# Optimization experiments

Hardware: AMD Instinct MI355X
Metric: run time of the kernel (lower is better)

Reference implementation:

```python
import jax, jax.numpy as jnp
import numpy as np

N_SRC, N_DST, N_EDGE, D = 100000, 40000, 600000, 128
LN_EPS = 1e-5

def _mlp(x, w1, b1, w2, b2, g, beta):
    # anemoi MLP: Linear -> SiLU -> Linear -> LayerNorm
    h = jax.nn.silu(x @ w1 + b1)
    h = h @ w2 + b2
    mu = jnp.mean(h, axis=-1, keepdims=True)
    var = jnp.var(h, axis=-1, keepdims=True)
    return (h - mu) * jax.lax.rsqrt(var + LN_EPS) * g + beta

def setup_inputs() -> dict:
    key = jax.random.key(0)
    ks = jax.random.split(key, 12)
    def rn(k, shape, scale):
        return jax.random.normal(k, shape, dtype=jnp.float32) * scale
    w_scale = 0.05
    return dict(
        x_src=rn(ks[0], (N_SRC, D), 1.0),
        x_dst=rn(ks[1], (N_DST, D), 1.0),
        edge_attr=rn(ks[2], (N_EDGE, D), 1.0),
        edge_index=jnp.stack([
            jax.random.randint(ks[3], (N_EDGE,), 0, N_SRC),
            jax.random.randint(ks[4], (N_EDGE,), 0, N_DST)]).astype(jnp.int32),
        edge_w1=rn(ks[5], (3 * D, D), w_scale), edge_b1=jnp.zeros((D,), jnp.float32),
        edge_w2=rn(ks[6], (D, D), w_scale), edge_b2=jnp.zeros((D,), jnp.float32),
        edge_g=jnp.ones((D,), jnp.float32), edge_beta=jnp.zeros((D,), jnp.float32),
        node_w1=rn(ks[7], (2 * D, D), w_scale), node_b1=jnp.zeros((D,), jnp.float32),
        node_w2=rn(ks[8], (D, D), w_scale), node_b2=jnp.zeros((D,), jnp.float32),
        node_g=jnp.ones((D,), jnp.float32), node_beta=jnp.zeros((D,), jnp.float32),
    )

def reference(x_src, x_dst, edge_attr, edge_index,
              edge_w1, edge_b1, edge_w2, edge_b2, edge_g, edge_beta,
              node_w1, node_b1, node_w2, node_b2, node_g, node_beta):
    src, dst = edge_index[0], edge_index[1]
    # GraphConv message: x_i = dst node feats, x_j = src node feats (PyG source_to_target)
    x_i = x_dst[dst]              # [E, D] gather
    x_j = x_src[src]              # [E, D] gather
    edges_new = _mlp(jnp.concatenate([x_i, x_j, edge_attr], axis=-1),
                     edge_w1, edge_b1, edge_w2, edge_b2, edge_g, edge_beta) + edge_attr
    # sum-aggregate messages to dst nodes (chunked sum == single sum)
    agg = jax.ops.segment_sum(edges_new, dst, num_segments=N_DST)  # [N_DST, D]
    nodes_new_dst = _mlp(jnp.concatenate([x_dst, agg], axis=-1),
                         node_w1, node_b1, node_w2, node_b2, node_g, node_beta) + x_dst
    # update_src_nodes=True branch
    nodes_new_src = _mlp(jnp.concatenate([x_src, x_src], axis=-1),
                         node_w1, node_b1, node_w2, node_b2, node_g, node_beta) + x_src
    return nodes_new_src, nodes_new_dst, edges_new
```

## Files before the change

### kernel.cpp

```cpp
#include <hip/hip_runtime.h>
#include <hip/hip_bf16.h>

#define NSRC  100000
#define NDST  40000
#define NEDGE 600000
#define AGG_BYTES   20480000ull
#define GB_BYTES    2048ull
#define W1F_OFF   (AGG_BYTES + GB_BYTES)
#define W2F_OFF   (W1F_OFF + 98304ull)
#define NW1F_OFF  (W2F_OFF + 32768ull)
#define NW2F_OFF  (NW1F_OFF + 65536ull)
#define NW1SF_OFF (NW2F_OFF + 32768ull)
#define WS_REQUIRED (NW1SF_OFF + 32768ull)

typedef __bf16 bf16;
typedef __attribute__((ext_vector_type(8))) __bf16 bf16x8;
typedef __attribute__((ext_vector_type(4))) float f32x4;

__device__ __forceinline__ unsigned short bfbits(float f) {
    return __builtin_bit_cast(unsigned short, (__bf16)f);
}

__device__ __forceinline__ f32x4 mfma16(bf16x8 a, bf16x8 b, f32x4 c) {
    return __builtin_amdgcn_mfma_f32_16x16x32_bf16(a, b, c, 0, 0, 0);
}

__device__ __forceinline__ bf16x8 pack8(float4 a, float4 b) {
    union { uint4 u; bf16x8 v; } o;
    o.u.x = (unsigned)bfbits(a.x) | ((unsigned)bfbits(a.y) << 16);
    o.u.y = (unsigned)bfbits(a.z) | ((unsigned)bfbits(a.w) << 16);
    o.u.z = (unsigned)bfbits(b.x) | ((unsigned)bfbits(b.y) << 16);
    o.u.w = (unsigned)bfbits(b.z) | ((unsigned)bfbits(b.w) << 16);
    return o.v;
}

__device__ __forceinline__ bf16x8 cvt8p(const float* p) {
    return pack8(*(const float4*)p, *(const float4*)(p + 4));
}

__device__ __forceinline__ void cvt8hl(const float* p, bf16x8& hi, bf16x8& lo) {
    float4 a = *(const float4*)p;
    float4 b = *(const float4*)(p + 4);
    float v[8] = {a.x, a.y, a.z, a.w, b.x, b.y, b.z, b.w};
    union { uint4 u; bf16x8 v; } H, L;
    unsigned hw[8], lw[8];
#pragma unroll
    for (int i = 0; i < 8; ++i) {
        bf16 h = (bf16)v[i];
        hw[i] = (unsigned)__builtin_bit_cast(unsigned short, h);
        lw[i] = (unsigned)bfbits(v[i] - (float)h);
    }
    H.u.x = hw[0] | (hw[1] << 16); H.u.y = hw[2] | (hw[3] << 16);
    H.u.z = hw[4] | (hw[5] << 16); H.u.w = hw[6] | (hw[7] << 16);
    L.u.x = lw[0] | (lw[1] << 16); L.u.y = lw[2] | (lw[3] << 16);
    L.u.z = lw[4] | (lw[5] << 16); L.u.w = lw[6] | (lw[7] << 16);
    hi = H.v; lo = L.v;
}

__global__ __launch_bounds__(256) void prep_kernel(
    const float* __restrict__ w1, const float* __restrict__ w2,
    const float* __restrict__ nw1, const float* __restrict__ nw2,
    bf16* __restrict__ w1f, bf16* __restrict__ w2f,
    bf16* __restrict__ nw1f, bf16* __restrict__ nw2f, bf16* __restrict__ nw1sf) {
    int i = blockIdx.x * 256 + threadIdx.x;
    if (i < 49152) {
        int j = i & 7, lane = (i >> 3) & 63, f = (i >> 9) & 3;
        int rest = i >> 11; int ks = rest % 12, wc = rest / 12;
        int k = ks * 32 + (lane >> 4) * 8 + j;
        int n = wc * 64 + f * 16 + (lane & 15);
        w1f[i] = (bf16)w1[k * 128 + n];
    } else if (i < 65536) {
        int q = i - 49152;
        int j = q & 7, lane = (q >> 3) & 63, f = (q >> 9) & 3;
        int rest = q >> 11; int ks = rest & 3, wc = rest >> 2;
        int k = ks * 32 + (lane >> 4) * 8 + j;
        int n = wc * 64 + f * 16 + (lane & 15);
        w2f[q] = (bf16)w2[k * 128 + n];
    } else if (i < 98304) {
        int q = i - 65536;
        int j = q & 7, lane = (q >> 3) & 63, f = (q >> 9) & 3;
        int rest = q >> 11; int ks = rest & 7, wc = rest >> 3;
        int k = ks * 32 + (lane >> 4) * 8 + j;
        int n = wc * 64 + f * 16 + (lane & 15);
        nw1f[q] = (bf16)nw1[k * 128 + n];
    } else if (i < 114688) {
        int q = i - 98304;
        int j = q & 7, lane = (q >> 3) & 63, f = (q >> 9) & 3;
        int rest = q >> 11; int ks = rest & 3, wc = rest >> 2;
        int k = ks * 32 + (lane >> 4) * 8 + j;
        int n = wc * 64 + f * 16 + (lane & 15);
        nw2f[q] = (bf16)nw2[k * 128 + n];
    } else {
        int q = i - 114688;
        int j = q & 7, lane = (q >> 3) & 63, f = (q >> 9) & 3;
        int rest = q >> 11; int ks = rest & 3, wc = rest >> 2;
        int k = ks * 32 + (lane >> 4) * 8 + j;
        int n = wc * 64 + f * 16 + (lane & 15);
        nw1sf[q] = (bf16)(nw1[k * 128 + n] + nw1[(k + 128) * 128 + n]);
    }
}

__global__ void select_gbeta(const float* __restrict__ a, const float* __restrict__ b,
                             float* __restrict__ g_out, float* __restrict__ beta_out) {
    int t = threadIdx.x;
    bool a_is_g = (a[0] == 1.0f);
    const float* g  = a_is_g ? a : b;
    const float* be = a_is_g ? b : a;
    g_out[t]    = g[t];
    beta_out[t] = be[t];
}

__device__ __forceinline__ void mlp_tail(
    f32x4 (&acc)[2][4], char* sH, float* redS, float* redQ,
    const bf16x8* w2v, const float* b1, const float* b2,
    const float* g, const float* be,
    int wr, int wc, int lr, int lg, int lane,
    float (&outv)[2][4][4])
{
    {
        float b1c[4];
#pragma unroll
        for (int fc = 0; fc < 4; ++fc) b1c[fc] = b1[wc * 64 + fc * 16 + lr];
#pragma unroll
        for (int fr = 0; fr < 2; ++fr)
#pragma unroll
            for (int fc = 0; fc < 4; ++fc)
#pragma unroll
                for (int rg = 0; rg < 4; ++rg) {
                    int row = wr * 32 + fr * 16 + lg * 4 + rg;
                    int col = wc * 64 + fc * 16 + lr;
                    float v = acc[fr][fc][rg] + b1c[fc];
                    v = v / (1.f + __expf(-v));
                    *(bf16*)(sH + ((row * 256 + col * 2) ^ ((row & 7) << 4))) = (bf16)v;
                }
    }
    __syncthreads();

#pragma unroll
    for (int i = 0; i < 2; ++i)
#pragma unroll
        for (int j = 0; j < 4; ++j) acc[i][j] = f32x4{0.f, 0.f, 0.f, 0.f};
#pragma unroll
    for (int ks = 0; ks < 4; ++ks) {
        bf16x8 a[2], b[4];
#pragma unroll
        for (int f = 0; f < 2; ++f) {
            int ra = wr * 32 + f * 16 + lr;
            a[f] = *(const bf16x8*)(sH + ((ra * 256 + ks * 64 + lg * 16) ^ ((ra & 7) << 4)));
        }
#pragma unroll
        for (int fc = 0; fc < 4; ++fc)
            b[fc] = w2v[((wc * 4 + ks) * 4 + fc) * 64 + lane];
#pragma unroll
        for (int i = 0; i < 2; ++i)
#pragma unroll
            for (int j = 0; j < 4; ++j)
                acc[i][j] = mfma16(a[i], b[j], acc[i][j]);
    }

    float b2c[4], gc[4], bc[4];
#pragma unroll
    for (int fc = 0; fc < 4; ++fc) {
        int col = wc * 64 + fc * 16 + lr;
        b2c[fc] = b2[col]; gc[fc] = g[col]; bc[fc] = be[col];
    }
#pragma unroll
    for (int fr = 0; fr < 2; ++fr)
#pragma unroll
        for (int rg = 0; rg < 4; ++rg) {
            float s = 0.f, sq = 0.f;
#pragma unroll
            for (int fc = 0; fc < 4; ++fc) {
                float v = acc[fr][fc][rg] + b2c[fc];
                acc[fr][fc][rg] = v;
                s += v; sq += v * v;
            }
#pragma unroll
            for (int m = 1; m < 16; m <<= 1) {
                s  += __shfl_xor(s, m, 64);
                sq += __shfl_xor(sq, m, 64);
            }
            if (lr == 0) {
                int row = wr * 32 + fr * 16 + lg * 4 + rg;
                redS[row * 2 + wc] = s;
                redQ[row * 2 + wc] = sq;
            }
        }
    __syncthreads();

#pragma unroll
    for (int fr = 0; fr < 2; ++fr)
#pragma unroll
        for (int rg = 0; rg < 4; ++rg) {
            int row = wr * 32 + fr * 16 + lg * 4 + rg;
            float s  = redS[row * 2] + redS[row * 2 + 1];
            float sq = redQ[row * 2] + redQ[row * 2 + 1];
            float mean = s * (1.f / 128.f);
            float var  = fmaxf(sq * (1.f / 128.f) - mean * mean, 0.f);
            float rstd = rsqrtf(var + 1e-5f);
#pragma unroll
            for (int fc = 0; fc < 4; ++fc)
                outv[fr][fc][rg] = (acc[fr][fc][rg] - mean) * rstd * gc[fc] + bc[fc];
        }
}

__global__ __launch_bounds__(256, 4) void edge_mfma(
    const float* __restrict__ xsrc, const float* __restrict__ xdst,
    const float* __restrict__ attr, const int* __restrict__ eidx,
    const bf16* __restrict__ w1f,  const bf16* __restrict__ w2f,
    const float* __restrict__ b1,  const float* __restrict__ b2,
    const float* __restrict__ g,   const float* __restrict__ be,
    float* __restrict__ oute, float* __restrict__ agg)
{
    __shared__ __align__(16) char sH[16384];
    __shared__ float redS[128], redQ[128];
    __shared__ int sS[64], sD[64];

    const int t = threadIdx.x;
    const long e0 = (long)blockIdx.x * 64;
    if (t < 64) {
        long e = e0 + t;
        sS[t] = min(max(eidx[e], 0), NSRC - 1);
        sD[t] = min(max(eidx[NEDGE + e], 0), NDST - 1);
    }
    __syncthreads();

    const int lane = t & 63, w = t >> 6;
    const int wr = w >> 1, wc = w & 1;
    const int lr = lane & 15, lg = lane >> 4;

    const int r0w = wr * 32 + lr, r1w = r0w + 16;
    const float* xi0 = xdst + (long)sD[r0w] * 128;
    const float* xi1 = xdst + (long)sD[r1w] * 128;
    const float* xj0 = xsrc + (long)sS[r0w] * 128;
    const float* xj1 = xsrc + (long)sS[r1w] * 128;
    const float* at0 = attr + (e0 + r0w) * 128;
    const float* at1 = attr + (e0 + r1w) * 128;

    const bf16x8* w1v = (const bf16x8*)w1f;
    const bf16x8* w2v = (const bf16x8*)w2f;

    f32x4 acc[2][4];
#pragma unroll
    for (int i = 0; i < 2; ++i)
#pragma unroll
        for (int j = 0; j < 4; ++j) acc[i][j] = f32x4{0.f, 0.f, 0.f, 0.f};

    float4 raw[3][2][2];
#define LOADKS(d_, ks_) { \
        const float* q0 = ((ks_) < 4 ? xi0 : (ks_) < 8 ? xj0 : at0) + (((ks_) & 3) * 32 + lg * 8); \
        const float* q1 = ((ks_) < 4 ? xi1 : (ks_) < 8 ? xj1 : at1) + (((ks_) & 3) * 32 + lg * 8); \
        raw[d_][0][0] = *(const float4*)q0; raw[d_][0][1] = *(const float4*)(q0 + 4); \
        raw[d_][1][0] = *(const float4*)q1; raw[d_][1][1] = *(const float4*)(q1 + 4); }

    LOADKS(0, 0) LOADKS(1, 1) LOADKS(2, 2)

#pragma unroll
    for (int ks = 0; ks < 12; ++ks) {
        const int d = ks % 3;
        bf16x8 a0 = pack8(raw[d][0][0], raw[d][0][1]);
        bf16x8 a1 = pack8(raw[d][1][0], raw[d][1][1]);
        if (ks + 3 < 12) { LOADKS(d, ks + 3) }
        bf16x8 b[4];
#pragma unroll
        for (int fc = 0; fc < 4; ++fc)
            b[fc] = w1v[((wc * 12 + ks) * 4 + fc) * 64 + lane];
#pragma unroll
        for (int j = 0; j < 4; ++j) {
            acc[0][j] = mfma16(a0, b[j], acc[0][j]);
            acc[1][j] = mfma16(a1, b[j], acc[1][j]);
        }
    }
#undef LOADKS

    float outv[2][4][4];
    mlp_tail(acc, sH, redS, redQ, w2v, b1, b2, g, be, wr, wc, lr, lg, lane, outv);

#pragma unroll
    for (int fr = 0; fr < 2; ++fr)
#pragma unroll
        for (int rg = 0; rg < 4; ++rg) {
            int row = wr * 32 + fr * 16 + lg * 4 + rg;
            long e = e0 + row;
            long dbase = (long)sD[row] * 128;
#pragma unroll
            for (int fc = 0; fc < 4; ++fc) {
                int col = wc * 64 + fc * 16 + lr;
                float v = outv[fr][fc][rg] + attr[e * 128 + col];
                __builtin_nontemporal_store(v, &oute[e * 128 + col]);
                atomicAdd(agg + dbase + col, v);
            }
        }
}

__global__ __launch_bounds__(256, 4) void node_src_mfma(
    const float* __restrict__ xsrc,
    const bf16* __restrict__ nw1sf, const bf16* __restrict__ nw2f,
    const float* __restrict__ b1, const float* __restrict__ b2,
    const float* __restrict__ g,  const float* __restrict__ be,
    float* __restrict__ outp)
{
    __shared__ __align__(16) char sH[16384];
    __shared__ float redS[128], redQ[128];

    const int t = threadIdx.x;
    const long r0 = (long)blockIdx.x * 64;
    const int lane = t & 63, w = t >> 6;
    const int wr = w >> 1, wc = w & 1;
    const int lr = lane & 15, lg = lane >> 4;

    long gr0 = r0 + wr * 32 + lr;      if (gr0 >= NSRC) gr0 = NSRC - 1;
    long gr1 = r0 + wr * 32 + 16 + lr; if (gr1 >= NSRC) gr1 = NSRC - 1;
    const float* x0 = xsrc + gr0 * 128;
    const float* x1 = xsrc + gr1 * 128;

    const bf16x8* w1v = (const bf16x8*)nw1sf;
    const bf16x8* w2v = (const bf16x8*)nw2f;

    f32x4 acc[2][4];
#pragma unroll
    for (int i = 0; i < 2; ++i)
#pragma unroll
        for (int j = 0; j < 4; ++j) acc[i][j] = f32x4{0.f, 0.f, 0.f, 0.f};

#pragma unroll
    for (int ks = 0; ks < 4; ++ks) {
        int k0 = ks * 32 + lg * 8;
        bf16x8 a0 = cvt8p(x0 + k0);
        bf16x8 a1 = cvt8p(x1 + k0);
        bf16x8 b[4];
#pragma unroll
        for (int fc = 0; fc < 4; ++fc)
            b[fc] = w1v[((wc * 4 + ks) * 4 + fc) * 64 + lane];
#pragma unroll
        for (int j = 0; j < 4; ++j) {
            acc[0][j] = mfma16(a0, b[j], acc[0][j]);
            acc[1][j] = mfma16(a1, b[j], acc[1][j]);
        }
    }

    float outv[2][4][4];
    mlp_tail(acc, sH, redS, redQ, w2v, b1, b2, g, be, wr, wc, lr, lg, lane, outv);

#pragma unroll
    for (int fr = 0; fr < 2; ++fr)
#pragma unroll
        for (int rg = 0; rg < 4; ++rg) {
            int row = wr * 32 + fr * 16 + lg * 4 + rg;
            long gr = r0 + row;
            if (gr < NSRC) {
#pragma unroll
                for (int fc = 0; fc < 4; ++fc) {
                    int col = wc * 64 + fc * 16 + lr;
                    float v = outv[fr][fc][rg] + xsrc[gr * 128 + col];
                    __builtin_nontemporal_store(v, &outp[gr * 128 + col]);
                }
            }
        }
}

__global__ __launch_bounds__(256, 4) void node_dst_mfma(
    const float* __restrict__ xdst, const float* __restrict__ agg,
    const bf16* __restrict__ nw1f, const bf16* __restrict__ nw2f,
    const float* __restrict__ b1, const float* __restrict__ b2,
    const float* __restrict__ g,  const float* __restrict__ be,
    float* __restrict__ outp)
{
    __shared__ __align__(16) char sH[16384];
    __shared__ float redS[128], redQ[128];

    const int t = threadIdx.x;
    const long r0 = (long)blockIdx.x * 64;
    const int lane = t & 63, w = t >> 6;
    const int wr = w >> 1, wc = w & 1;
    const int lr = lane & 15, lg = lane >> 4;

    long gr0 = r0 + wr * 32 + lr;
    long gr1 = gr0 + 16;
    const float* x0 = xdst + gr0 * 128;
    const float* x1 = xdst + gr1 * 128;
    const float* a0p = agg + gr0 * 128;
    const float* a1p = agg + gr1 * 128;

    const bf16x8* w1v = (const bf16x8*)nw1f;
    const bf16x8* w2v = (const bf16x8*)nw2f;

    f32x4 acc[2][4];
#pragma unroll
    for (int i = 0; i < 2; ++i)
#pragma unroll
        for (int j = 0; j < 4; ++j) acc[i][j] = f32x4{0.f, 0.f, 0.f, 0.f};

#pragma unroll
    for (int ks = 0; ks < 4; ++ks) {
        int k0 = ks * 32 + lg * 8;
        bf16x8 a0 = cvt8p(x0 + k0);
        bf16x8 a1 = cvt8p(x1 + k0);
        bf16x8 b[4];
#pragma unroll
        for (int fc = 0; fc < 4; ++fc)
            b[fc] = w1v[((wc * 8 + ks) * 4 + fc) * 64 + lane];
#pragma unroll
        for (int j = 0; j < 4; ++j) {
            acc[0][j] = mfma16(a0, b[j], acc[0][j]);
            acc[1][j] = mfma16(a1, b[j], acc[1][j]);
        }
    }
#pragma unroll
    for (int ks = 0; ks < 4; ++ks) {
        int k0 = ks * 32 + lg * 8;
        bf16x8 h0, l0, h1, l1;
        cvt8hl(a0p + k0, h0, l0);
        cvt8hl(a1p + k0, h1, l1);
        bf16x8 b[4];
#pragma unroll
        for (int fc = 0; fc < 4; ++fc)
            b[fc] = w1v[((wc * 8 + 4 + ks) * 4 + fc) * 64 + lane];
#pragma unroll
        for (int j = 0; j < 4; ++j) {
            acc[0][j] = mfma16(h0, b[j], acc[0][j]);
            acc[1][j] = mfma16(h1, b[j], acc[1][j]);
            acc[0][j] = mfma16(l0, b[j], acc[0][j]);
            acc[1][j] = mfma16(l1, b[j], acc[1][j]);
        }
    }

    float outv[2][4][4];
    mlp_tail(acc, sH, redS, redQ, w2v, b1, b2, g, be, wr, wc, lr, lg, lane, outv);

#pragma unroll
    for (int fr = 0; fr < 2; ++fr)
#pragma unroll
        for (int rg = 0; rg < 4; ++rg) {
            int row = wr * 32 + fr * 16 + lg * 4 + rg;
            long gr = r0 + row;
#pragma unroll
            for (int fc = 0; fc < 4; ++fc) {
                int col = wc * 64 + fc * 16 + lr;
                float v = outv[fr][fc][rg] + xdst[gr * 128 + col];
                __builtin_nontemporal_store(v, &outp[gr * 128 + col]);
            }
        }
}

extern "C" void kernel_launch(void* const* d_in, const int* in_sizes, int n_in,
                              void* d_out, int out_size, void* d_ws, size_t ws_size,
                              hipStream_t stream) {
    if (ws_size < WS_REQUIRED) return;

    const float* xsrc = nullptr; const float* xdst = nullptr;
    const float* attr = nullptr; const int*   eidx = nullptr;
    const float* ew1  = nullptr; const float* nw1  = nullptr;
    const float* w2s[2] = {nullptr, nullptr}; int n16384 = 0;
    const float* v128[8] = {nullptr}; int n128 = 0;

    for (int i = 0; i < n_in; ++i) {
        switch (in_sizes[i]) {
            case 12800000: xsrc = (const float*)d_in[i]; break;
            case 5120000:  xdst = (const float*)d_in[i]; break;
            case 76800000: attr = (const float*)d_in[i]; break;
            case 1200000:  eidx = (const int*)d_in[i];   break;
            case 49152:    ew1  = (const float*)d_in[i]; break;
            case 32768:    nw1  = (const float*)d_in[i]; break;
            case 16384:    if (n16384 < 2) w2s[n16384++] = (const float*)d_in[i]; break;
            case 128:      if (n128 < 8)   v128[n128++]  = (const float*)d_in[i]; break;
            default: break;
        }
    }
    if (!xsrc || !xdst || !attr || !eidx || !ew1 || !nw1 || n16384 != 2 || n128 != 8)
        return;

    const float* ew2 = w2s[0];
    const float* nw2 = w2s[1];
    const float* eb1 = v128[0]; const float* eb2 = v128[1];
    const float* egA = v128[2]; const float* egB = v128[3];
    const float* nb1 = v128[4]; const float* nb2 = v128[5];
    const float* ngA = v128[6]; const float* ngB = v128[7];

    char* ws = (char*)d_ws;
    float* agg  = (float*)ws;
    float* egv  = (float*)(ws + AGG_BYTES);
    float* ebv  = egv + 128;
    float* ngv  = ebv + 128;
    float* nbv  = ngv + 128;
    bf16* w1f   = (bf16*)(ws + W1F_OFF);
    bf16* w2f   = (bf16*)(ws + W2F_OFF);
    bf16* nw1f  = (bf16*)(ws + NW1F_OFF);
    bf16* nw2f  = (bf16*)(ws + NW2F_OFF);
    bf16* nw1sf = (bf16*)(ws + NW1SF_OFF);

    float* out      = (float*)d_out;
    float* out_src  = out;
    float* out_dst  = out + (long)NSRC * 128;
    float* out_edge = out + (long)(NSRC + NDST) * 128;

    hipMemsetAsync(agg, 0, (size_t)NDST * 128 * sizeof(float), stream);
    select_gbeta<<<1, 128, 0, stream>>>(egA, egB, egv, ebv);
    select_gbeta<<<1, 128, 0, stream>>>(ngA, ngB, ngv, nbv);
    prep_kernel<<<512, 256, 0, stream>>>(ew1, ew2, nw1, nw2, w1f, w2f, nw1f, nw2f, nw1sf);

    edge_mfma<<<NEDGE / 64, 256, 0, stream>>>(
        xsrc, xdst, attr, eidx, w1f, w2f, eb1, eb2, egv, ebv, out_edge, agg);
    node_src_mfma<<<(NSRC + 63) / 64, 256, 0, stream>>>(
        xsrc, nw1sf, nw2f, nb1, nb2, ngv, nbv, out_src);
    node_dst_mfma<<<NDST / 64, 256, 0, stream>>>(
        xdst, agg, nw1f, nw2f, nb1, nb2, ngv, nbv, out_dst);
}
```

Before: 607.5 us.

## Replace atomic scatter-add aggregation with CSR gather in node_dst kernel

The edge kernel no longer does float atomicAdds into a global aggregation buffer. Instead, a histogram, single-block scan and scatter build a CSR list of edges per destination node. The node_dst kernel then gathers and sums edge outputs into shared memory before its MLP. This removes 77M atomics and the 20MB memset, at the cost of three extra kernels, a serial scan, and a random re-read of the edge output (307MB). Stores also switch from nontemporal to regular so edge outputs may stay in cache for the gather.

```diff
diff --git a/kernel.cpp b/kernel.cpp
--- a/kernel.cpp
+++ b/kernel.cpp
@@ -4,14 +4,18 @@
 #define NSRC  100000
 #define NDST  40000
 #define NEDGE 600000
-#define AGG_BYTES   20480000ull
-#define GB_BYTES    2048ull
-#define W1F_OFF   (AGG_BYTES + GB_BYTES)
-#define W2F_OFF   (W1F_OFF + 98304ull)
-#define NW1F_OFF  (W2F_OFF + 32768ull)
-#define NW2F_OFF  (NW1F_OFF + 65536ull)
-#define NW1SF_OFF (NW2F_OFF + 32768ull)
-#define WS_REQUIRED (NW1SF_OFF + 32768ull)
+
+#define GB_OFF     0ull
+#define W1F_OFF    2048ull
+#define W2F_OFF    (W1F_OFF + 98304ull)
+#define NW1F_OFF   (W2F_OFF + 32768ull)
+#define NW2F_OFF   (NW1F_OFF + 65536ull)
+#define NW1SF_OFF  (NW2F_OFF + 32768ull)
+#define DEG_OFF    (NW1SF_OFF + 32768ull)
+#define CSR_OFF    (DEG_OFF + 160000ull)
+#define CUR_OFF    (CSR_OFF + 160016ull)
+#define CE_OFF     (CUR_OFF + 160000ull)
+#define WS_REQUIRED (CE_OFF + 2400000ull)
 
 typedef __bf16 bf16;
 typedef __attribute__((ext_vector_type(8))) __bf16 bf16x8;
@@ -38,9 +42,7 @@
     return pack8(*(const float4*)p, *(const float4*)(p + 4));
 }
 
-__device__ __forceinline__ void cvt8hl(const float* p, bf16x8& hi, bf16x8& lo) {
-    float4 a = *(const float4*)p;
-    float4 b = *(const float4*)(p + 4);
+__device__ __forceinline__ void cvt8hl_v(float4 a, float4 b, bf16x8& hi, bf16x8& lo) {
     float v[8] = {a.x, a.y, a.z, a.w, b.x, b.y, b.z, b.w};
     union { uint4 u; bf16x8 v; } H, L;
     unsigned hw[8], lw[8];
@@ -110,6 +112,57 @@
     beta_out[t] = be[t];
 }
 
+__global__ __launch_bounds__(256) void hist_kernel(const int* __restrict__ eidx,
+                                                   int* __restrict__ deg) {
+    int e = blockIdx.x * 256 + threadIdx.x;
+    if (e < NEDGE) {
+        int d = min(max(eidx[NEDGE + e], 0), NDST - 1);
+        atomicAdd(&deg[d], 1);
+    }
+}
+
+__global__ __launch_bounds__(1024) void scan_kernel(const int* __restrict__ deg,
+                                                    int* __restrict__ csr,
+                                                    int* __restrict__ cur) {
+    __shared__ int buf[1024];
+    __shared__ int carry;
+    int t = threadIdx.x;
+    if (t == 0) carry = 0;
+    __syncthreads();
+    for (int base = 0; base < NDST; base += 1024) {
+        int i = base + t;
+        int v = (i < NDST) ? deg[i] : 0;
+        buf[t] = v;
+        __syncthreads();
+        for (int off = 1; off < 1024; off <<= 1) {
+            int add = (t >= off) ? buf[t - off] : 0;
+            __syncthreads();
+            buf[t] += add;
+            __syncthreads();
+        }
+        if (i < NDST) {
+            int excl = carry + buf[t] - v;
+            csr[i] = excl;
+            cur[i] = excl;
+        }
+        __syncthreads();
+        if (t == 0) carry += buf[1023];
+        __syncthreads();
+    }
+    if (t == 0) csr[NDST] = NEDGE;
+}
+
+__global__ __launch_bounds__(256) void scatter_kernel(const int* __restrict__ eidx,
+                                                      int* __restrict__ cur,
+                                                      int* __restrict__ ce) {
+    int e = blockIdx.x * 256 + threadIdx.x;
+    if (e < NEDGE) {
+        int d = min(max(eidx[NEDGE + e], 0), NDST - 1);
+        int pos = atomicAdd(&cur[d], 1);
+        ce[pos] = e;
+    }
+}
+
 __device__ __forceinline__ void mlp_tail(
     f32x4 (&acc)[2][4], char* sH, float* redS, float* redQ,
     const bf16x8* w2v, const float* b1, const float* b2,
@@ -210,7 +263,7 @@
     const bf16* __restrict__ w1f,  const bf16* __restrict__ w2f,
     const float* __restrict__ b1,  const float* __restrict__ b2,
     const float* __restrict__ g,   const float* __restrict__ be,
-    float* __restrict__ oute, float* __restrict__ agg)
+    float* __restrict__ oute)
 {
     __shared__ __align__(16) char sH[16384];
     __shared__ float redS[128], redQ[128];
@@ -282,13 +335,11 @@
         for (int rg = 0; rg < 4; ++rg) {
             int row = wr * 32 + fr * 16 + lg * 4 + rg;
             long e = e0 + row;
-            long dbase = (long)sD[row] * 128;
 #pragma unroll
             for (int fc = 0; fc < 4; ++fc) {
                 int col = wc * 64 + fc * 16 + lr;
                 float v = outv[fr][fc][rg] + attr[e * 128 + col];
-                __builtin_nontemporal_store(v, &oute[e * 128 + col]);
-                atomicAdd(agg + dbase + col, v);
+                oute[e * 128 + col] = v;
             }
         }
 }
@@ -352,20 +403,21 @@
 #pragma unroll
                 for (int fc = 0; fc < 4; ++fc) {
                     int col = wc * 64 + fc * 16 + lr;
-                    float v = outv[fr][fc][rg] + xsrc[gr * 128 + col];
-                    __builtin_nontemporal_store(v, &outp[gr * 128 + col]);
+                    outp[gr * 128 + col] = outv[fr][fc][rg] + xsrc[gr * 128 + col];
                 }
             }
         }
 }
 
-__global__ __launch_bounds__(256, 4) void node_dst_mfma(
-    const float* __restrict__ xdst, const float* __restrict__ agg,
+__global__ __launch_bounds__(256, 3) void node_dst_mfma(
+    const float* __restrict__ xdst, const float* __restrict__ oute,
+    const int* __restrict__ csr, const int* __restrict__ ce,
     const bf16* __restrict__ nw1f, const bf16* __restrict__ nw2f,
     const float* __restrict__ b1, const float* __restrict__ b2,
     const float* __restrict__ g,  const float* __restrict__ be,
     float* __restrict__ outp)
 {
+    __shared__ __align__(16) char sAgg[32768];
     __shared__ __align__(16) char sH[16384];
     __shared__ float redS[128], redQ[128];
 
@@ -375,12 +427,31 @@
     const int wr = w >> 1, wc = w & 1;
     const int lr = lane & 15, lg = lane >> 4;
 
+    for (int rr = 0; rr < 16; ++rr) {
+        int row = w * 16 + rr;
+        long gr = r0 + row;
+        int s0 = csr[gr], s1 = csr[gr + 1];
+        float ax = 0.f, ay = 0.f, az = 0.f, aw2 = 0.f;
+        for (int i = s0 + (lane >> 5); i < s1; i += 2) {
+            int e = ce[i];
+            float4 vv = *(const float4*)(oute + (long)e * 128 + (lane & 31) * 4);
+            ax += vv.x; ay += vv.y; az += vv.z; aw2 += vv.w;
+        }
+        ax  += __shfl_xor(ax, 32);
+        ay  += __shfl_xor(ay, 32);
+        az  += __shfl_xor(az, 32);
+        aw2 += __shfl_xor(aw2, 32);
+        if (lane < 32) {
+            float4 o; o.x = ax; o.y = ay; o.z = az; o.w = aw2;
+            *(float4*)(sAgg + ((row * 512 + (lane & 31) * 16) ^ ((row & 7) << 4))) = o;
+        }
+    }
+    __syncthreads();
+
     long gr0 = r0 + wr * 32 + lr;
     long gr1 = gr0 + 16;
     const float* x0 = xdst + gr0 * 128;
     const float* x1 = xdst + gr1 * 128;
-    const float* a0p = agg + gr0 * 128;
-    const float* a1p = agg + gr1 * 128;
 
     const bf16x8* w1v = (const bf16x8*)nw1f;
     const bf16x8* w2v = (const bf16x8*)nw2f;
@@ -406,12 +477,18 @@
             acc[1][j] = mfma16(a1, b[j], acc[1][j]);
         }
     }
+    const int rowl0 = wr * 32 + lr, rowl1 = rowl0 + 16;
 #pragma unroll
     for (int ks = 0; ks < 4; ++ks) {
-        int k0 = ks * 32 + lg * 8;
+        int base0 = rowl0 * 512 + ks * 128 + lg * 32;
+        int base1 = rowl1 * 512 + ks * 128 + lg * 32;
+        float4 aA = *(const float4*)(sAgg + ((base0)      ^ ((rowl0 & 7) << 4)));
+        float4 aB = *(const float4*)(sAgg + ((base0 + 16) ^ ((rowl0 & 7) << 4)));
+        float4 bA = *(const float4*)(sAgg + ((base1)      ^ ((rowl1 & 7) << 4)));
+        float4 bB = *(const float4*)(sAgg + ((base1 + 16) ^ ((rowl1 & 7) << 4)));
         bf16x8 h0, l0, h1, l1;
-        cvt8hl(a0p + k0, h0, l0);
-        cvt8hl(a1p + k0, h1, l1);
+        cvt8hl_v(aA, aB, h0, l0);
+        cvt8hl_v(bA, bB, h1, l1);
         bf16x8 b[4];
 #pragma unroll
         for (int fc = 0; fc < 4; ++fc)
@@ -437,8 +514,7 @@
 #pragma unroll
             for (int fc = 0; fc < 4; ++fc) {
                 int col = wc * 64 + fc * 16 + lr;
-                float v = outv[fr][fc][rg] + xdst[gr * 128 + col];
-                __builtin_nontemporal_store(v, &outp[gr * 128 + col]);
+                outp[gr * 128 + col] = outv[fr][fc][rg] + xdst[gr * 128 + col];
             }
         }
 }
@@ -478,8 +554,7 @@
     const float* ngA = v128[6]; const float* ngB = v128[7];
 
     char* ws = (char*)d_ws;
-    float* agg  = (float*)ws;
-    float* egv  = (float*)(ws + AGG_BYTES);
+    float* egv  = (float*)(ws + GB_OFF);
     float* ebv  = egv + 128;
     float* ngv  = ebv + 128;
     float* nbv  = ngv + 128;
@@ -488,21 +563,29 @@
     bf16* nw1f  = (bf16*)(ws + NW1F_OFF);
     bf16* nw2f  = (bf16*)(ws + NW2F_OFF);
     bf16* nw1sf = (bf16*)(ws + NW1SF_OFF);
+    int*  deg   = (int*)(ws + DEG_OFF);
+    int*  csr   = (int*)(ws + CSR_OFF);
+    int*  cur   = (int*)(ws + CUR_OFF);
+    int*  ce    = (int*)(ws + CE_OFF);
 
     float* out      = (float*)d_out;
     float* out_src  = out;
     float* out_dst  = out + (long)NSRC * 128;
     float* out_edge = out + (long)(NSRC + NDST) * 128;
 
-    hipMemsetAsync(agg, 0, (size_t)NDST * 128 * sizeof(float), stream);
+    hipMemsetAsync(deg, 0, (size_t)NDST * sizeof(int), stream);
     select_gbeta<<<1, 128, 0, stream>>>(egA, egB, egv, ebv);
     select_gbeta<<<1, 128, 0, stream>>>(ngA, ngB, ngv, nbv);
     prep_kernel<<<512, 256, 0, stream>>>(ew1, ew2, nw1, nw2, w1f, w2f, nw1f, nw2f, nw1sf);
 
+    hist_kernel<<<(NEDGE + 255) / 256, 256, 0, stream>>>(eidx, deg);
+    scan_kernel<<<1, 1024, 0, stream>>>(deg, csr, cur);
+    scatter_kernel<<<(NEDGE + 255) / 256, 256, 0, stream>>>(eidx, cur, ce);
+
     edge_mfma<<<NEDGE / 64, 256, 0, stream>>>(
-        xsrc, xdst, attr, eidx, w1f, w2f, eb1, eb2, egv, ebv, out_edge, agg);
+        xsrc, xdst, attr, eidx, w1f, w2f, eb1, eb2, egv, ebv, out_edge);
     node_src_mfma<<<(NSRC + 63) / 64, 256, 0, stream>>>(
         xsrc, nw1sf, nw2f, nb1, nb2, ngv, nbv, out_src);
     node_dst_mfma<<<NDST / 64, 256, 0, stream>>>(
-        xdst, agg, nw1f, nw2f, nb1, nb2, ngv, nbv, out_dst);
-}
+        xdst, out_edge, csr, ce, nw1f, nw2f, nb1, nb2, ngv, nbv, out_dst);
+}
```

After: 728.1 us. 19.9% more time.
